# Optimization experiments

Measured on AMD Instinct MI355X. Metric: run time of the kernel, lower is better.

Reference implementation:

```python
import jax, jax.numpy as jnp
import numpy as np

EPS = 1e-14
RHO = 8.0


def _normalize(x):
    return x / jnp.linalg.norm(x, axis=-1, keepdims=True)


def setup_inputs() -> dict:
    key = jax.random.key(0)
    ks = jax.random.split(key, 12)
    B, D = 4096, 1024
    f = lambda k: _normalize(jax.random.normal(k, (B, D), dtype=jnp.float32))
    pos = lambda k: jax.random.uniform(k, (B, 1), dtype=jnp.float32, minval=0.1, maxval=1.0)
    return {
        "im_feat": f(ks[0]),
        "tt_feat": f(ks[1]),
        "rim_feat": f(ks[2]),
        "rtt_feat": f(ks[3]),
        "remote_u_im": pos(ks[4]),
        "remote_u_tt": pos(ks[5]),
        "loss1_im": pos(ks[6]),
        "loss1_tt": pos(ks[7]),
        "u_im": pos(ks[8]),
        "u_tt": pos(ks[9]),
        "logit_scale": 10.0 * jnp.ones((1,), dtype=jnp.float32),
        "offset": 0,
    }


def _pairwise_loss(rim, rtt, im, tt, logit_scale, offset):
    # features1 = remote, features2 = local (as in forward(): pairwise_loss(remote_features, features, ...))
    sim_image = rim @ tt.T                                  # [B1, B2]
    sim_text = rtt @ im.T                                   # [B1, B2]
    diag_sim = jnp.sum(rim * rtt, axis=-1, keepdims=True)   # [B1, 1]
    exp_im = jnp.exp((sim_image - diag_sim) * logit_scale)
    exp_tt = jnp.exp((sim_text - diag_sim) * logit_scale)
    B1, B2 = sim_image.shape
    # mask zeros the shifted diagonal: equivalent to subtracting the diagonal entry from the row sum
    cols = (jnp.arange(B1) + offset)[:, None]               # [B1, 1]
    rw_sum = B2 - 1 if B1 <= B2 else B2 * (B1 - 1) / B1
    loss_im = (jnp.sum(exp_im, axis=-1, keepdims=True)
               - jnp.take_along_axis(exp_im, cols, axis=1)) / rw_sum
    loss_tt = (jnp.sum(exp_tt, axis=-1, keepdims=True)
               - jnp.take_along_axis(exp_tt, cols, axis=1)) / rw_sum
    return loss_im, loss_tt


def reference(im_feat, tt_feat, rim_feat, rtt_feat, remote_u_im, remote_u_tt,
              loss1_im, loss1_tt, u_im, u_tt, logit_scale, offset):
    loss2_im, loss2_tt = _pairwise_loss(rim_feat, rtt_feat, im_feat, tt_feat, logit_scale, offset)
    pg1 = loss1_im / (u_im + EPS) + loss1_tt / (u_tt + EPS)
    pg2 = loss2_im / (remote_u_im + EPS) + loss2_tt / (remote_u_tt + EPS)
    loss = (jnp.mean(pg1) + jnp.mean(pg2)) / 2
    # multiply_tau branch
    ls = logit_scale[0]
    loss = loss / jax.lax.stop_gradient(ls)
    loss = loss + RHO / ls
    loss = loss + jnp.mean(jnp.log(u_im) + jnp.log(u_tt)) / 2 / ls
    return loss
```

## Files before the change

### kernel.cpp

```cpp
#include <hip/hip_runtime.h>
#include <hip/hip_bf16.h>

#define EPSF 1e-14f
#define RHOF 8.0f

typedef __attribute__((ext_vector_type(4))) float f32x4;
typedef __attribute__((ext_vector_type(8))) int   i32x8;

#define AS_GLOBAL __attribute__((address_space(1)))
#define AS_LDS    __attribute__((address_space(3)))


__global__ __launch_bounds__(256) void prep_fp8(
    const float* __restrict__ im,  const float* __restrict__ tt,
    const float* __restrict__ rim, const float* __restrict__ rtt,
    unsigned char* __restrict__ bIm,  unsigned char* __restrict__ bTt,
    unsigned char* __restrict__ bRim, unsigned char* __restrict__ bRtt,
    float* __restrict__ S_im, float* __restrict__ S_tt,
    float* __restrict__ diag, float* __restrict__ red,
    int D, int bpm )
{
    const int b = blockIdx.x;
    const int tid = threadIdx.x;
    const int nConv = 4 * bpm;
    if (b < nConv) {
        int mIdx = b / bpm;
        int blk  = b - mIdx * bpm;
        const float* src = (mIdx == 0) ? rim : (mIdx == 1) ? tt
                          : (mIdx == 2) ? rtt : im;
        unsigned char* dst = (mIdx == 0) ? bRim : (mIdx == 1) ? bTt
                            : (mIdx == 2) ? bRtt : bIm;
        const int upr = D >> 4;
        const int rpb = 256 / upr;
        const int urow = tid / upr;
        const int c    = tid - urow * upr;
        const int r    = blk * rpb + urow;
        const int kTiles = D >> 7;
        const float* p = src + (size_t)r * D + (size_t)c * 16;
        float4 v0 = ((const float4*)p)[0];
        float4 v1 = ((const float4*)p)[1];
        float4 v2 = ((const float4*)p)[2];
        float4 v3 = ((const float4*)p)[3];
        int w0 = __builtin_amdgcn_cvt_pk_fp8_f32(v0.x, v0.y, 0, false);
        w0     = __builtin_amdgcn_cvt_pk_fp8_f32(v0.z, v0.w, w0, true);
        int w1 = __builtin_amdgcn_cvt_pk_fp8_f32(v1.x, v1.y, 0, false);
        w1     = __builtin_amdgcn_cvt_pk_fp8_f32(v1.z, v1.w, w1, true);
        int w2 = __builtin_amdgcn_cvt_pk_fp8_f32(v2.x, v2.y, 0, false);
        w2     = __builtin_amdgcn_cvt_pk_fp8_f32(v2.z, v2.w, w2, true);
        int w3 = __builtin_amdgcn_cvt_pk_fp8_f32(v3.x, v3.y, 0, false);
        w3     = __builtin_amdgcn_cvt_pk_fp8_f32(v3.z, v3.w, w3, true);
        int4 out = make_int4(w0, w1, w2, w3);
        const int kb = c >> 3;
        const int p8 = (c & 7) ^ (r & 7);
        *(int4*)(dst + ((size_t)((r >> 7) * kTiles + kb) * 1024
                        + (size_t)(r & 127) * 8 + p8) * 16) = out;
    } else {
        int db = b - nConv;
        if (db == 0 && tid < 8) red[tid] = 0.f;
        if (tid < 4) { S_im[db * 4 + tid] = 0.f; S_tt[db * 4 + tid] = 0.f; }
        int row  = db * 4 + (tid >> 6);
        int lane = tid & 63;
        const float* a = rim + (size_t)row * D;
        const float* c2 = rtt + (size_t)row * D;
        float s = 0.f;
        for (int k = lane * 4; k < D; k += 256) {
            float4 av = *(const float4*)(a + k);
            float4 cv = *(const float4*)(c2 + k);
            s += av.x * cv.x + av.y * cv.y + av.z * cv.z + av.w * cv.w;
        }
        #pragma unroll
        for (int m2 = 1; m2 < 64; m2 <<= 1) s += __shfl_xor(s, m2, 64);
        if (lane == 0) diag[row] = s;
    }
}

__global__ __launch_bounds__(512, 2) void gemm_expsum(
    const unsigned char* __restrict__ A0, const unsigned char* __restrict__ B0,
    float* __restrict__ S0,
    const unsigned char* __restrict__ A1, const unsigned char* __restrict__ B1,
    float* __restrict__ S1,
    const float* __restrict__ logit_scale, const int* __restrict__ offset,
    int Bn, int D)
{
    __shared__ unsigned char As[2][32768];
    __shared__ unsigned char Bs[2][32768];

    const int tid  = threadIdx.x;
    const int wave = tid >> 6;
    const int lane = tid & 63;
    const int lo   = lane & 15;
    const int qd   = lane >> 4;
    const int wm   = wave >> 2;
    const int wn   = wave & 3;
    const int offA = ((2 * qd) ^ (lo & 7)) * 16;

    const int nx  = gridDim.x;
    const int nwg = nx * gridDim.y;
    int wg = blockIdx.y * nx + blockIdx.x;
    int swz = ((nwg & 7) == 0) ? ((wg & 7) * (nwg >> 3) + (wg >> 3)) : wg;
    const int by = swz / nx;
    const int bx = swz - by * nx;

    const int kTiles = D >> 7;

    const int half = wave >> 1;
    const int part = wave & 1;
    const bool ownerIsA = (half < 2);
    const int ownerLoff = (half & 1) * 16384 + part * 8192;

    auto stageOwner = [&](int buf, const unsigned char* At,
                          const unsigned char* Bt, int kb) {
        const unsigned char* g =
            (ownerIsA ? At + (size_t)half * kTiles * 16384
                      : Bt + (size_t)(half - 2) * kTiles * 16384)
            + (size_t)kb * 16384 + part * 8192 + lane * 16;
        unsigned char* l = (ownerIsA ? &As[buf][0] : &Bs[buf][0]) + ownerLoff;
        #pragma unroll
        for (int q = 0; q < 8; ++q)
            __builtin_amdgcn_global_load_lds(
                (const AS_GLOBAL unsigned int*)(g + q * 1024),
                (AS_LDS unsigned int*)(l + q * 1024), 16, 0, 0);
    };

    const int aOff0 = wm * 16384 + lo * 128 + offA;
    const int bOff0 = (wn >> 1) * 16384 + ((wn & 1) * 64 + lo) * 128 + offA;

    const float ls = logit_scale[0];
    const int offs = offset[0];

    for (int zz = 0; zz < 2; ++zz) {
        const unsigned char* A = zz ? A1 : A0;
        const unsigned char* B = zz ? B1 : B0;
        float* S = zz ? S1 : S0;
        const unsigned char* Atile = A + (size_t)(2 * by) * kTiles * 16384;
        const unsigned char* Btile = B + (size_t)(2 * bx) * kTiles * 16384;

        f32x4 acc[8][4];
        #pragma unroll
        for (int i = 0; i < 8; ++i)
            #pragma unroll
            for (int j = 0; j < 4; ++j)
                acc[i][j] = (f32x4){0.f, 0.f, 0.f, 0.f};

        if (zz == 0) {
            stageOwner(0, Atile, Btile, 0);
            asm volatile("s_waitcnt vmcnt(0)" ::: "memory");
            __builtin_amdgcn_s_barrier();
        }

        for (int kb = 0; kb < kTiles; ++kb) {
            const int cur = kb & 1;
            if (kb + 1 < kTiles) {
                stageOwner(1 - cur, Atile, Btile, kb + 1);
            } else if (zz == 0) {
                stageOwner(1 - cur,
                           A1 + (size_t)(2 * by) * kTiles * 16384,
                           B1 + (size_t)(2 * bx) * kTiles * 16384, 0);
            }

            i32x8 bq[4];
            #pragma unroll
            for (int tj = 0; tj < 4; ++tj) {
                const int ba = bOff0 + tj * 2048;
                union { int4 h[2]; i32x8 v; } u;
                u.h[0] = *(const int4*)&Bs[cur][ba];
                u.h[1] = *(const int4*)&Bs[cur][ba ^ 16];
                bq[tj] = u.v;
            }

            #pragma unroll
            for (int ph = 0; ph < 4; ++ph) {
                const int ti0 = 2 * ph;
                union { int4 h[2]; i32x8 v; } ua0, ua1;
                {
                    const int aa0 = aOff0 + ti0 * 2048;
                    ua0.h[0] = *(const int4*)&As[cur][aa0];
                    ua0.h[1] = *(const int4*)&As[cur][aa0 ^ 16];
                    const int aa1 = aOff0 + (ti0 + 1) * 2048;
                    ua1.h[0] = *(const int4*)&As[cur][aa1];
                    ua1.h[1] = *(const int4*)&As[cur][aa1 ^ 16];
                }
                #pragma unroll
                for (int tj = 0; tj < 4; ++tj)
                    acc[ti0][tj] = __builtin_amdgcn_mfma_scale_f32_16x16x128_f8f6f4(
                        ua0.v, bq[tj], acc[ti0][tj],
                        0, 0, 0, 127, 0, 127);
                #pragma unroll
                for (int tj = 0; tj < 4; ++tj)
                    acc[ti0 + 1][tj] = __builtin_amdgcn_mfma_scale_f32_16x16x128_f8f6f4(
                        ua1.v, bq[tj], acc[ti0 + 1][tj],
                        0, 0, 0, 127, 0, 127);
            }

            if (kb + 1 < kTiles) {
                asm volatile("s_waitcnt vmcnt(0)" ::: "memory");
                __builtin_amdgcn_s_barrier();
            }
        }

        const int rowBase = by * 256 + wm * 128;
        const int colBase = bx * 256 + wn * 64;
        #pragma unroll
        for (int ti = 0; ti < 8; ++ti) {
            #pragma unroll
            for (int r = 0; r < 4; ++r) {
                int gi = rowBase + 16 * ti + 4 * qd + r;
                float rs = 0.f;
                #pragma unroll
                for (int tj = 0; tj < 4; ++tj) {
                    int gj = colBase + 16 * tj + lo;
                    float e = __expf(ls * acc[ti][tj][r]);
                    if (gj == gi + offs) e = 0.f;
                    rs += e;
                }
                #pragma unroll
                for (int m = 1; m < 16; m <<= 1) rs += __shfl_xor(rs, m, 64);
                if (lo == 0) atomicAdd(&S[gi], rs);
            }
        }

        if (zz == 0) {
            asm volatile("s_waitcnt vmcnt(0)" ::: "memory");
            __builtin_amdgcn_s_barrier();
        }
    }
}

__global__ __launch_bounds__(256) void final_kernel(
    const float* __restrict__ S_im, const float* __restrict__ S_tt,
    const float* __restrict__ diag,
    const float* __restrict__ ru_im, const float* __restrict__ ru_tt,
    const float* __restrict__ l1_im, const float* __restrict__ l1_tt,
    const float* __restrict__ u_im,  const float* __restrict__ u_tt,
    const float* __restrict__ logit_scale, float* __restrict__ red,
    float* __restrict__ out, int Bn)
{
    const float ls = logit_scale[0];
    const float inv_rw = 1.0f / (float)(Bn - 1);
    const int gid = blockIdx.x * 256 + threadIdx.x;
    const int stride = gridDim.x * 256;
    float pg = 0.f, lg = 0.f;
    for (int i = gid; i < Bn; i += stride) {
        float p1 = l1_im[i] / (u_im[i] + EPSF) + l1_tt[i] / (u_tt[i] + EPSF);
        float dd = expf(-ls * diag[i]);
        float p2 = dd * S_im[i] * inv_rw / (ru_im[i] + EPSF)
                 + dd * S_tt[i] * inv_rw / (ru_tt[i] + EPSF);
        pg += p1 + p2;
        lg += logf(u_im[i]) + logf(u_tt[i]);
    }
    __shared__ float sp[256], sl[256];
    sp[threadIdx.x] = pg; sl[threadIdx.x] = lg;
    __syncthreads();
    for (int s = 128; s > 0; s >>= 1) {
        if (threadIdx.x < s) { sp[threadIdx.x] += sp[threadIdx.x + s];
                               sl[threadIdx.x] += sl[threadIdx.x + s]; }
        __syncthreads();
    }
    if (threadIdx.x == 0) {
        atomicAdd(&red[0], sp[0]);
        atomicAdd(&red[1], sl[0]);
        __threadfence();
        int t = atomicAdd((int*)&red[2], 1);
        if (t == gridDim.x - 1) {
            float pgSum = atomicAdd(&red[0], 0.f);
            float lgSum = atomicAdd(&red[1], 0.f);
            float loss = ((pgSum / (float)Bn) * 0.5f) / ls
                       + RHOF / ls
                       + (lgSum / (float)Bn) * 0.5f / ls;
            out[0] = loss;
        }
    }
}

extern "C" void kernel_launch(void* const* d_in, const int* in_sizes, int n_in,
                              void* d_out, int out_size, void* d_ws, size_t ws_size,
                              hipStream_t stream) {
    const float* im    = (const float*)d_in[0];
    const float* tt    = (const float*)d_in[1];
    const float* rim   = (const float*)d_in[2];
    const float* rtt   = (const float*)d_in[3];
    const float* ru_im = (const float*)d_in[4];
    const float* ru_tt = (const float*)d_in[5];
    const float* l1_im = (const float*)d_in[6];
    const float* l1_tt = (const float*)d_in[7];
    const float* u_im  = (const float*)d_in[8];
    const float* u_tt  = (const float*)d_in[9];
    const float* lsc   = (const float*)d_in[10];
    const int*   offs  = (const int*)d_in[11];

    const int Bn = in_sizes[4];
    const int D  = in_sizes[0] / Bn;
    const int rpb = 4096 / D;
    const int bpm = Bn / rpb;

    char* base = (char*)d_ws;
    float* S_im = (float*)base;
    float* S_tt = S_im + Bn;
    float* diag = S_tt + Bn;
    float* red  = diag + Bn;
    const size_t headBytes = (((size_t)(3 * Bn + 8) * sizeof(float)) + 255) & ~(size_t)255;
    const size_t matBytes  = (size_t)Bn * D;
    unsigned char* buf0 = (unsigned char*)(base + headBytes);
    unsigned char* bRim = buf0;
    unsigned char* bTt  = buf0 + matBytes;
    unsigned char* bRtt = buf0 + 2 * matBytes;
    unsigned char* bIm  = buf0 + 3 * matBytes;

    prep_fp8<<<4 * bpm + Bn / 4, 256, 0, stream>>>(
        im, tt, rim, rtt, bIm, bTt, bRim, bRtt, S_im, S_tt, diag, red, D, bpm);

    dim3 ggrid(Bn / 256, Bn / 256, 1);
    gemm_expsum<<<ggrid, 512, 0, stream>>>(bRim, bTt, S_im, bRtt, bIm, S_tt,
                                           lsc, offs, Bn, D);

    final_kernel<<<32, 256, 0, stream>>>(S_im, S_tt, diag, ru_im, ru_tt,
                                         l1_im, l1_tt, u_im, u_tt, lsc,
                                         red, (float*)d_out, Bn);
}
```

Baseline: 174.3 us.

## Load B operand directly from global into registers, dropping B LDS buffers

Replaces LDS staging of the B tile with per-wave direct global loads into registers, prefetched one k-tile ahead and double-buffered in registers. A staging is redistributed across all 8 waves. This halves LDS usage and removes the LDS reads for B, at the cost of more global/L2 traffic, since waves sharing a B column each fetch it, and of more register pressure from the extra prefetch buffers. It also risks occupancy loss under launch_bounds(512,2).

```diff
diff --git a/kernel.cpp b/kernel.cpp
--- a/kernel.cpp
+++ b/kernel.cpp
@@ -83,7 +83,6 @@
     int Bn, int D)
 {
     __shared__ unsigned char As[2][32768];
-    __shared__ unsigned char Bs[2][32768];
 
     const int tid  = threadIdx.x;
     const int wave = tid >> 6;
@@ -103,30 +102,39 @@
 
     const int kTiles = D >> 7;
 
-    const int half = wave >> 1;
-    const int part = wave & 1;
-    const bool ownerIsA = (half < 2);
-    const int ownerLoff = (half & 1) * 16384 + part * 8192;
-
-    auto stageOwner = [&](int buf, const unsigned char* At,
-                          const unsigned char* Bt, int kb) {
-        const unsigned char* g =
-            (ownerIsA ? At + (size_t)half * kTiles * 16384
-                      : Bt + (size_t)(half - 2) * kTiles * 16384)
-            + (size_t)kb * 16384 + part * 8192 + lane * 16;
-        unsigned char* l = (ownerIsA ? &As[buf][0] : &Bs[buf][0]) + ownerLoff;
-        #pragma unroll
-        for (int q = 0; q < 8; ++q)
+    const int sh = wave >> 2;
+    const int sq = wave & 3;
+    auto stageA = [&](int buf, const unsigned char* At, int kb) {
+        const unsigned char* g = At + ((size_t)sh * kTiles + kb) * 16384
+                               + sq * 4096 + lane * 16;
+        #pragma unroll
+        for (int q = 0; q < 4; ++q)
             __builtin_amdgcn_global_load_lds(
                 (const AS_GLOBAL unsigned int*)(g + q * 1024),
-                (AS_LDS unsigned int*)(l + q * 1024), 16, 0, 0);
+                (AS_LDS unsigned int*)&As[buf][wave * 4096 + q * 1024],
+                16, 0, 0);
     };
 
+    const size_t bRowOff = (size_t)(((wn & 1) * 64 + lo) * 128 + offA);
+    auto loadB = [&](i32x8* dst, const unsigned char* Bt, int kb) {
+        const unsigned char* g = Bt + ((size_t)(wn >> 1) * kTiles + kb) * 16384
+                               + bRowOff;
+        #pragma unroll
+        for (int tj = 0; tj < 4; ++tj) {
+            union { int4 h[2]; i32x8 v; } u;
+            const unsigned char* gp = g + tj * 2048;
+            u.h[0] = *(const int4*)gp;
+            u.h[1] = *(const int4*)((const unsigned char*)((size_t)gp ^ 16));
+            dst[tj] = u.v;
+        }
+    };
+
     const int aOff0 = wm * 16384 + lo * 128 + offA;
-    const int bOff0 = (wn >> 1) * 16384 + ((wn & 1) * 64 + lo) * 128 + offA;
 
     const float ls = logit_scale[0];
     const int offs = offset[0];
+
+    i32x8 bq[4], bqN[4];
 
     for (int zz = 0; zz < 2; ++zz) {
         const unsigned char* A = zz ? A1 : A0;
@@ -143,7 +151,8 @@
                 acc[i][j] = (f32x4){0.f, 0.f, 0.f, 0.f};
 
         if (zz == 0) {
-            stageOwner(0, Atile, Btile, 0);
+            stageA(0, Atile, 0);
+            loadB(bq, Btile, 0);
             asm volatile("s_waitcnt vmcnt(0)" ::: "memory");
             __builtin_amdgcn_s_barrier();
         }
@@ -151,21 +160,11 @@
         for (int kb = 0; kb < kTiles; ++kb) {
             const int cur = kb & 1;
             if (kb + 1 < kTiles) {
-                stageOwner(1 - cur, Atile, Btile, kb + 1);
+                stageA(1 - cur, Atile, kb + 1);
+                loadB(bqN, Btile, kb + 1);
             } else if (zz == 0) {
-                stageOwner(1 - cur,
-                           A1 + (size_t)(2 * by) * kTiles * 16384,
-                           B1 + (size_t)(2 * bx) * kTiles * 16384, 0);
-            }
-
-            i32x8 bq[4];
-            #pragma unroll
-            for (int tj = 0; tj < 4; ++tj) {
-                const int ba = bOff0 + tj * 2048;
-                union { int4 h[2]; i32x8 v; } u;
-                u.h[0] = *(const int4*)&Bs[cur][ba];
-                u.h[1] = *(const int4*)&Bs[cur][ba ^ 16];
-                bq[tj] = u.v;
+                stageA(1 - cur, A1 + (size_t)(2 * by) * kTiles * 16384, 0);
+                loadB(bqN, B1 + (size_t)(2 * bx) * kTiles * 16384, 0);
             }
 
             #pragma unroll
@@ -195,6 +194,10 @@
             if (kb + 1 < kTiles) {
                 asm volatile("s_waitcnt vmcnt(0)" ::: "memory");
                 __builtin_amdgcn_s_barrier();
+            }
+            if (kb + 1 < kTiles || zz == 0) {
+                #pragma unroll
+                for (int j = 0; j < 4; ++j) bq[j] = bqN[j];
             }
         }
 
```

Result: slower. 295.9 us (+69.8%).

## Shrink GEMM tiles to 128x128, split both GEMMs across grid z, drop double buffering

Applied to the files above, without the earlier changes.

The fused FP8 GEMM+exp-sum kernel moves from 512-thread blocks computing 256x256 tiles for both similarity matrices in sequence to 256-thread blocks computing 128x128 tiles, with the two matrices split across blockIdx.z. The double-buffered LDS prefetch pipeline is replaced by single-buffered load/sync/compute/sync. This cuts LDS and registers per block so more blocks can be resident, and makes the grid much larger. In exchange it loses load/compute overlap and roughly doubles global traffic per FLOP because of the lower data reuse.

```diff
diff --git a/kernel.cpp b/kernel.cpp
--- a/kernel.cpp
+++ b/kernel.cpp
@@ -74,7 +74,7 @@
     }
 }
 
-__global__ __launch_bounds__(512, 2) void gemm_expsum(
+__global__ __launch_bounds__(256) void gemm_expsum(
     const unsigned char* __restrict__ A0, const unsigned char* __restrict__ B0,
     float* __restrict__ S0,
     const unsigned char* __restrict__ A1, const unsigned char* __restrict__ B1,
@@ -82,16 +82,21 @@
     const float* __restrict__ logit_scale, const int* __restrict__ offset,
     int Bn, int D)
 {
-    __shared__ unsigned char As[2][32768];
-    __shared__ unsigned char Bs[2][32768];
+    __shared__ unsigned char As[16384];
+    __shared__ unsigned char Bs[16384];
+
+    const int z = blockIdx.z;
+    const unsigned char* A = z ? A1 : A0;
+    const unsigned char* B = z ? B1 : B0;
+    float* S = z ? S1 : S0;
 
     const int tid  = threadIdx.x;
     const int wave = tid >> 6;
     const int lane = tid & 63;
     const int lo   = lane & 15;
     const int qd   = lane >> 4;
-    const int wm   = wave >> 2;
-    const int wn   = wave & 3;
+    const int wm   = wave >> 1;
+    const int wn   = wave & 1;
     const int offA = ((2 * qd) ^ (lo & 7)) * 16;
 
     const int nx  = gridDim.x;
@@ -102,126 +107,86 @@
     const int bx = swz - by * nx;
 
     const int kTiles = D >> 7;
-
-    const int half = wave >> 1;
-    const int part = wave & 1;
-    const bool ownerIsA = (half < 2);
-    const int ownerLoff = (half & 1) * 16384 + part * 8192;
-
-    auto stageOwner = [&](int buf, const unsigned char* At,
-                          const unsigned char* Bt, int kb) {
-        const unsigned char* g =
-            (ownerIsA ? At + (size_t)half * kTiles * 16384
-                      : Bt + (size_t)(half - 2) * kTiles * 16384)
-            + (size_t)kb * 16384 + part * 8192 + lane * 16;
-        unsigned char* l = (ownerIsA ? &As[buf][0] : &Bs[buf][0]) + ownerLoff;
-        #pragma unroll
-        for (int q = 0; q < 8; ++q)
-            __builtin_amdgcn_global_load_lds(
-                (const AS_GLOBAL unsigned int*)(g + q * 1024),
-                (AS_LDS unsigned int*)(l + q * 1024), 16, 0, 0);
-    };
-
-    const int aOff0 = wm * 16384 + lo * 128 + offA;
-    const int bOff0 = (wn >> 1) * 16384 + ((wn & 1) * 64 + lo) * 128 + offA;
+    const unsigned char* Atile = A + (size_t)by * kTiles * 16384;
+    const unsigned char* Btile = B + (size_t)bx * kTiles * 16384;
+
+    f32x4 acc[4][4];
+    #pragma unroll
+    for (int i = 0; i < 4; ++i)
+        #pragma unroll
+        for (int j = 0; j < 4; ++j)
+            acc[i][j] = (f32x4){0.f, 0.f, 0.f, 0.f};
+
+    const int aOff0 = (wm * 64 + lo) * 128 + offA;
+    const int bOff0 = (wn * 64 + lo) * 128 + offA;
+
+    for (int kb = 0; kb < kTiles; ++kb) {
+        {
+            const unsigned char* Ag = Atile + (size_t)kb * 16384
+                                    + wave * 4096 + lane * 16;
+            const unsigned char* Bg = Btile + (size_t)kb * 16384
+                                    + wave * 4096 + lane * 16;
+            #pragma unroll
+            for (int q = 0; q < 4; ++q) {
+                __builtin_amdgcn_global_load_lds(
+                    (const AS_GLOBAL unsigned int*)(Ag + q * 1024),
+                    (AS_LDS unsigned int*)&As[wave * 4096 + q * 1024],
+                    16, 0, 0);
+                __builtin_amdgcn_global_load_lds(
+                    (const AS_GLOBAL unsigned int*)(Bg + q * 1024),
+                    (AS_LDS unsigned int*)&Bs[wave * 4096 + q * 1024],
+                    16, 0, 0);
+            }
+        }
+        __syncthreads();
+
+        i32x8 bq[4];
+        #pragma unroll
+        for (int tj = 0; tj < 4; ++tj) {
+            const int ba = bOff0 + tj * 2048;
+            union { int4 h[2]; i32x8 v; } u;
+            u.h[0] = *(const int4*)&Bs[ba];
+            u.h[1] = *(const int4*)&Bs[ba ^ 16];
+            bq[tj] = u.v;
+        }
+        #pragma unroll
+        for (int ti = 0; ti < 4; ++ti) {
+            const int aa = aOff0 + ti * 2048;
+            union { int4 h[2]; i32x8 v; } u;
+            u.h[0] = *(const int4*)&As[aa];
+            u.h[1] = *(const int4*)&As[aa ^ 16];
+            i32x8 af = u.v;
+            #pragma unroll
+            for (int tj = 0; tj < 4; ++tj)
+                acc[ti][tj] = __builtin_amdgcn_mfma_scale_f32_16x16x128_f8f6f4(
+                    af, bq[tj], acc[ti][tj],
+                    0, 0,
+                    0, 127,
+                    0, 127);
+        }
+        __syncthreads();
+    }
 
     const float ls = logit_scale[0];
     const int offs = offset[0];
-
-    for (int zz = 0; zz < 2; ++zz) {
-        const unsigned char* A = zz ? A1 : A0;
-        const unsigned char* B = zz ? B1 : B0;
-        float* S = zz ? S1 : S0;
-        const unsigned char* Atile = A + (size_t)(2 * by) * kTiles * 16384;
-        const unsigned char* Btile = B + (size_t)(2 * bx) * kTiles * 16384;
-
-        f32x4 acc[8][4];
-        #pragma unroll
-        for (int i = 0; i < 8; ++i)
-            #pragma unroll
-            for (int j = 0; j < 4; ++j)
-                acc[i][j] = (f32x4){0.f, 0.f, 0.f, 0.f};
-
-        if (zz == 0) {
-            stageOwner(0, Atile, Btile, 0);
-            asm volatile("s_waitcnt vmcnt(0)" ::: "memory");
-            __builtin_amdgcn_s_barrier();
-        }
-
-        for (int kb = 0; kb < kTiles; ++kb) {
-            const int cur = kb & 1;
-            if (kb + 1 < kTiles) {
-                stageOwner(1 - cur, Atile, Btile, kb + 1);
-            } else if (zz == 0) {
-                stageOwner(1 - cur,
-                           A1 + (size_t)(2 * by) * kTiles * 16384,
-                           B1 + (size_t)(2 * bx) * kTiles * 16384, 0);
+    const int rowBase = by * 128 + wm * 64;
+    const int colBase = bx * 128 + wn * 64;
+    #pragma unroll
+    for (int ti = 0; ti < 4; ++ti) {
+        #pragma unroll
+        for (int r = 0; r < 4; ++r) {
+            int gi = rowBase + 16 * ti + 4 * qd + r;
+            float rs = 0.f;
+            #pragma unroll
+            for (int tj = 0; tj < 4; ++tj) {
+                int gj = colBase + 16 * tj + lo;
+                float e = __expf(ls * acc[ti][tj][r]);
+                if (gj == gi + offs) e = 0.f;
+                rs += e;
             }
-
-            i32x8 bq[4];
-            #pragma unroll
-            for (int tj = 0; tj < 4; ++tj) {
-                const int ba = bOff0 + tj * 2048;
-                union { int4 h[2]; i32x8 v; } u;
-                u.h[0] = *(const int4*)&Bs[cur][ba];
-                u.h[1] = *(const int4*)&Bs[cur][ba ^ 16];
-                bq[tj] = u.v;
-            }
-
-            #pragma unroll
-            for (int ph = 0; ph < 4; ++ph) {
-                const int ti0 = 2 * ph;
-                union { int4 h[2]; i32x8 v; } ua0, ua1;
-                {
-                    const int aa0 = aOff0 + ti0 * 2048;
-                    ua0.h[0] = *(const int4*)&As[cur][aa0];
-                    ua0.h[1] = *(const int4*)&As[cur][aa0 ^ 16];
-                    const int aa1 = aOff0 + (ti0 + 1) * 2048;
-                    ua1.h[0] = *(const int4*)&As[cur][aa1];
-                    ua1.h[1] = *(const int4*)&As[cur][aa1 ^ 16];
-                }
-                #pragma unroll
-                for (int tj = 0; tj < 4; ++tj)
-                    acc[ti0][tj] = __builtin_amdgcn_mfma_scale_f32_16x16x128_f8f6f4(
-                        ua0.v, bq[tj], acc[ti0][tj],
-                        0, 0, 0, 127, 0, 127);
-                #pragma unroll
-                for (int tj = 0; tj < 4; ++tj)
-                    acc[ti0 + 1][tj] = __builtin_amdgcn_mfma_scale_f32_16x16x128_f8f6f4(
-                        ua1.v, bq[tj], acc[ti0 + 1][tj],
-                        0, 0, 0, 127, 0, 127);
-            }
-
-            if (kb + 1 < kTiles) {
-                asm volatile("s_waitcnt vmcnt(0)" ::: "memory");
-                __builtin_amdgcn_s_barrier();
-            }
-        }
-
-        const int rowBase = by * 256 + wm * 128;
-        const int colBase = bx * 256 + wn * 64;
-        #pragma unroll
-        for (int ti = 0; ti < 8; ++ti) {
-            #pragma unroll
-            for (int r = 0; r < 4; ++r) {
-                int gi = rowBase + 16 * ti + 4 * qd + r;
-                float rs = 0.f;
-                #pragma unroll
-                for (int tj = 0; tj < 4; ++tj) {
-                    int gj = colBase + 16 * tj + lo;
-                    float e = __expf(ls * acc[ti][tj][r]);
-                    if (gj == gi + offs) e = 0.f;
-                    rs += e;
-                }
-                #pragma unroll
-                for (int m = 1; m < 16; m <<= 1) rs += __shfl_xor(rs, m, 64);
-                if (lo == 0) atomicAdd(&S[gi], rs);
-            }
-        }
-
-        if (zz == 0) {
-            asm volatile("s_waitcnt vmcnt(0)" ::: "memory");
-            __builtin_amdgcn_s_barrier();
+            #pragma unroll
+            for (int m = 1; m < 16; m <<= 1) rs += __shfl_xor(rs, m, 64);
+            if (lo == 0) atomicAdd(&S[gi], rs);
         }
     }
 }
@@ -309,8 +274,8 @@
     prep_fp8<<<4 * bpm + Bn / 4, 256, 0, stream>>>(
         im, tt, rim, rtt, bIm, bTt, bRim, bRtt, S_im, S_tt, diag, red, D, bpm);
 
-    dim3 ggrid(Bn / 256, Bn / 256, 1);
-    gemm_expsum<<<ggrid, 512, 0, stream>>>(bRim, bTt, S_im, bRtt, bIm, S_tt,
+    dim3 ggrid(Bn / 128, Bn / 128, 2);
+    gemm_expsum<<<ggrid, 256, 0, stream>>>(bRim, bTt, S_im, bRtt, bIm, S_tt,
                                            lsc, offs, Bn, D);
 
     final_kernel<<<32, 256, 0, stream>>>(S_im, S_tt, diag, ru_im, ru_tt,
```

Result: slower. 178.2 us (+2.2%).
